# Optimization experiments

Measured on AMD Instinct MI355X. Metric: run time of the kernel, lower is better.

Reference implementation:

```python
import jax, jax.numpy as jnp
import numpy as np

C = 768      # n_embd
H = 12       # n_head
L = 6        # n_layer (per stack: base and head)
BS = 256     # block_size (per-stream length t)
B = 2        # batch
VU = 512     # vocab_size_up
VD = 512     # vocab_size_down
NM = 438     # n_music


def _ln(x, g, b, eps=1e-5):
    m = jnp.mean(x, -1, keepdims=True)
    v = jnp.mean((x - m) ** 2, -1, keepdims=True)
    return (x - m) * jax.lax.rsqrt(v + eps) * g + b


def _blocks(x, p, mask):
    # p: tuple of 16 stacked [L, ...] param arrays; scan over layers
    def body(x, lp):
        g1, b1, Wq, Bq, Wk, Bk, Wv, Bv, Wo, Bo, g2, b2, Wf, Bf, Wp, Bp = lp
        Bb, T, Cc = x.shape
        D = Cc // H
        h = _ln(x, g1, b1)
        q = (h @ Wq + Bq).reshape(Bb, T, H, D).transpose(0, 2, 1, 3)
        k = (h @ Wk + Bk).reshape(Bb, T, H, D).transpose(0, 2, 1, 3)
        v = (h @ Wv + Bv).reshape(Bb, T, H, D).transpose(0, 2, 1, 3)
        att = jnp.einsum('bhid,bhjd->bhij', q, k) * (1.0 / np.sqrt(D).astype(np.float32))
        att = jnp.where(mask, att, jnp.float32(-1e9))
        att = jax.nn.softmax(att, axis=-1)
        y = jnp.einsum('bhij,bhjd->bhid', att, v).transpose(0, 2, 1, 3).reshape(Bb, T, Cc)
        x = x + y @ Wo + Bo
        h2 = _ln(x, g2, b2)
        x = x + jax.nn.gelu(h2 @ Wf + Bf, approximate=False) @ Wp + Bp
        return x, None
    x, _ = jax.lax.scan(body, x, p)
    return x


def _forward(idx_up, idx_down, cond, tok_emb_up, tok_emb_down, pos_emb, cond_w, cond_b,
             base_p, head_p, ln_f_g, ln_f_b, head_up_w, head_down_w):
    t = idx_up.shape[1]
    te = jnp.concatenate([cond @ cond_w + cond_b, tok_emb_up[idx_up], tok_emb_down[idx_down]], axis=1)
    pe = jnp.concatenate([pos_emb[:, :t], pos_emb[:, BS:BS + t], pos_emb[:, 2 * BS:2 * BS + t]], axis=1)
    x = te + pe  # [B, 3t, C]
    tril = jnp.tril(jnp.ones((t, t), bool))
    mask = jnp.tile(tril, (3, 3))[None, None]  # 3x3 tiled block-causal mask [1,1,3t,3t]
    x = _blocks(x, base_p, mask)
    x = _blocks(x, head_p, mask)
    x = _ln(x, ln_f_g, ln_f_b)
    logits_up = x[:, t:2 * t] @ head_up_w
    logits_down = x[:, 2 * t:3 * t] @ head_down_w
    return logits_up, logits_down


def setup_inputs() -> dict:
    key = jax.random.key(0)
    ks = iter(jax.random.split(key, 100))
    def nrm(shape):
        return 0.02 * jax.random.normal(next(ks), shape, jnp.float32)
    inp = {
        'idx_up': jax.random.randint(next(ks), (B, BS), 0, VU),
        'idx_down': jax.random.randint(next(ks), (B, BS), 0, VD),
        'cond': jax.random.normal(next(ks), (B, BS, NM), jnp.float32),
        'tok_emb_up': nrm((VU, C)),
        'tok_emb_down': nrm((VD, C)),
        'pos_emb': nrm((1, 3 * BS, C)),
        'cond_w': nrm((NM, C)),
        'cond_b': jnp.zeros((C,), jnp.float32),
    }
    for pre in ('base_', 'head_'):
        inp[pre + 'ln1_g'] = jnp.ones((L, C), jnp.float32)
        inp[pre + 'ln1_b'] = jnp.zeros((L, C), jnp.float32)
        inp[pre + 'wq'] = nrm((L, C, C)); inp[pre + 'bq'] = jnp.zeros((L, C), jnp.float32)
        inp[pre + 'wk'] = nrm((L, C, C)); inp[pre + 'bk'] = jnp.zeros((L, C), jnp.float32)
        inp[pre + 'wv'] = nrm((L, C, C)); inp[pre + 'bv'] = jnp.zeros((L, C), jnp.float32)
        inp[pre + 'wo'] = nrm((L, C, C)); inp[pre + 'bo'] = jnp.zeros((L, C), jnp.float32)
        inp[pre + 'ln2_g'] = jnp.ones((L, C), jnp.float32)
        inp[pre + 'ln2_b'] = jnp.zeros((L, C), jnp.float32)
        inp[pre + 'fc_w'] = nrm((L, C, 4 * C)); inp[pre + 'fc_b'] = jnp.zeros((L, 4 * C), jnp.float32)
        inp[pre + 'pr_w'] = nrm((L, 4 * C, C)); inp[pre + 'pr_b'] = jnp.zeros((L, C), jnp.float32)
    inp['ln_f_g'] = jnp.ones((C,), jnp.float32)
    inp['ln_f_b'] = jnp.zeros((C,), jnp.float32)
    inp['head_up_w'] = nrm((C, VU))
    inp['head_down_w'] = nrm((C, VD))
    return inp


def reference(idx_up, idx_down, cond, tok_emb_up, tok_emb_down, pos_emb, cond_w, cond_b,
              base_ln1_g, base_ln1_b, base_wq, base_bq, base_wk, base_bk, base_wv, base_bv,
              base_wo, base_bo, base_ln2_g, base_ln2_b, base_fc_w, base_fc_b, base_pr_w, base_pr_b,
              head_ln1_g, head_ln1_b, head_wq, head_bq, head_wk, head_bk, head_wv, head_bv,
              head_wo, head_bo, head_ln2_g, head_ln2_b, head_fc_w, head_fc_b, head_pr_w, head_pr_b,
              ln_f_g, ln_f_b, head_up_w, head_down_w):
    base_p = (base_ln1_g, base_ln1_b, base_wq, base_bq, base_wk, base_bk, base_wv, base_bv,
              base_wo, base_bo, base_ln2_g, base_ln2_b, base_fc_w, base_fc_b, base_pr_w, base_pr_b)
    head_p = (head_ln1_g, head_ln1_b, head_wq, head_bq, head_wk, head_bk, head_wv, head_bv,
              head_wo, head_bo, head_ln2_g, head_ln2_b, head_fc_w, head_fc_b, head_pr_w, head_pr_b)
    return _forward(idx_up, idx_down, cond, tok_emb_up, tok_emb_down, pos_emb, cond_w, cond_b,
                    base_p, head_p, ln_f_g, ln_f_b, head_up_w, head_down_w)
```

## Files before the change

kernel.cpp:

```cpp
#include <hip/hip_runtime.h>
#include <cmath>

typedef unsigned short u16;
typedef __bf16 bf16x8 __attribute__((ext_vector_type(8)));
typedef float f32x4 __attribute__((ext_vector_type(4)));
typedef float f32x16 __attribute__((ext_vector_type(16)));
typedef u16 u16x4 __attribute__((ext_vector_type(4)));
typedef u16 u16x2 __attribute__((ext_vector_type(2)));

#define GLOAD16(g, l) __builtin_amdgcn_global_load_lds( \
    (const __attribute__((address_space(1))) unsigned int*)(g), \
    (__attribute__((address_space(3))) unsigned int*)(l), 16, 0, 0)

__device__ __forceinline__ u16 f2b(float f) {
  unsigned u = __builtin_bit_cast(unsigned, f);
  unsigned r = (u + 0x7fffu + ((u >> 16) & 1u)) >> 16;
  return (u16)r;
}

__device__ __forceinline__ int xcd_swz(int lin, int nwg) {
  int q = nwg >> 3, r = nwg & 7;
  int xcd = lin & 7, idx = lin >> 3;
  return xcd * q + (xcd < r ? xcd : r) + idx;
}

__device__ __forceinline__ void trans_tile(const float* __restrict__ W, u16* __restrict__ Wo,
                                           int K, int N, int Kp, int n0, int k0)
{
  __shared__ float t[32][33];
  int tx = threadIdx.x & 31, ty = threadIdx.x >> 5;
  #pragma unroll
  for (int i = 0; i < 4; ++i) {
    int k = k0 + ty + i * 8;
    t[ty + i * 8][tx] = (k < K) ? W[(long)k * N + n0 + tx] : 0.0f;
  }
  __syncthreads();
  #pragma unroll
  for (int i = 0; i < 2; ++i) {
    int p = threadIdx.x + 256 * i;
    int nl = p >> 4, kk = (p & 15) * 2;
    u16x2 o2; o2[0] = f2b(t[kk][nl]); o2[1] = f2b(t[kk + 1][nl]);
    *(u16x2*)(Wo + (long)(n0 + nl) * Kp + k0 + kk) = o2;
  }
}

__global__ __launch_bounds__(256)
void transall_k(const float* wq0, const float* wk0, const float* wv0, const float* wo0,
                const float* fc0, const float* pr0,
                const float* wq1, const float* wk1, const float* wv1, const float* wo1,
                const float* fc1, const float* pr1,
                const float* hu, const float* hd, const float* cw,
                u16* qkvt, u16* wot, u16* fct, u16* prt, u16* hutd, u16* cwt)
{
  int bid = blockIdx.x;
  const float* src; u16* dst; int K, N, Kp, t, tilesX;
  if (bid < 82944) {
    int l = bid / 6912, local = bid - l * 6912;
    int s = l / 6, li = l - s * 6;
    if (local < 1728) {
      int p = local / 576; t = local - p * 576;
      const float* base = (p == 0) ? (s ? wq1 : wq0) : (p == 1) ? (s ? wk1 : wk0) : (s ? wv1 : wv0);
      src = base + (size_t)li * 768 * 768;
      dst = qkvt + (size_t)l * 2304 * 768 + (size_t)p * 768 * 768;
      K = 768; N = 768; Kp = 768; tilesX = 24;
    } else if (local < 2304) {
      t = local - 1728;
      src = (s ? wo1 : wo0) + (size_t)li * 768 * 768;
      dst = wot + (size_t)l * 768 * 768;
      K = 768; N = 768; Kp = 768; tilesX = 24;
    } else if (local < 4608) {
      t = local - 2304;
      src = (s ? fc1 : fc0) + (size_t)li * 768 * 3072;
      dst = fct + (size_t)l * 3072 * 768;
      K = 768; N = 3072; Kp = 768; tilesX = 96;
    } else {
      t = local - 4608;
      src = (s ? pr1 : pr0) + (size_t)li * 3072 * 768;
      dst = prt + (size_t)l * 768 * 3072;
      K = 3072; N = 768; Kp = 3072; tilesX = 24;
    }
  } else {
    int e = bid - 82944;
    if (e < 384)      { t = e;       src = hu; dst = hutd;             K = 768; N = 512; Kp = 768; tilesX = 16; }
    else if (e < 768) { t = e - 384; src = hd; dst = hutd + 512 * 768; K = 768; N = 512; Kp = 768; tilesX = 16; }
    else              { t = e - 768; src = cw; dst = cwt;              K = 438; N = 768; Kp = 448; tilesX = 24; }
  }
  int n0 = (t % tilesX) * 32, k0 = (t / tilesX) * 32;
  trans_tile(src, dst, K, N, Kp, n0, k0);
}

__global__ __launch_bounds__(256)
void transw_k(const float* __restrict__ W, u16* __restrict__ Wt,
              int K, int N, int Kp, long sIn, long sOut)
{
  int l = blockIdx.z;
  trans_tile(W + (long)l * sIn, Wt + (long)l * sOut, K, N, Kp, blockIdx.x * 32, blockIdx.y * 32);
}

__global__ void biascat_k(const float* bq0, const float* bk0, const float* bv0,
                          const float* bq1, const float* bk1, const float* bv1, float* o)
{
  int idx = blockIdx.x * 256 + threadIdx.x;
  int c = idx % 2304, l = idx / 2304;
  int st = l / 6, li = l % 6;
  const float* src = (c < 768) ? (st ? bq1 : bq0) : (c < 1536) ? (st ? bk1 : bk0) : (st ? bv1 : bv0);
  o[idx] = src[li * 768 + (c % 768)];
}

__global__ void condcvt_k(const float* __restrict__ c, u16* __restrict__ o)
{
  int idx = blockIdx.x * 256 + threadIdx.x;
  int k = idx % 448, r = idx / 448;
  o[idx] = f2b(k < 438 ? c[r * 438 + k] : 0.0f);
}

__global__ void embed_k(const int* __restrict__ iu, const int* __restrict__ idn,
                        const float* __restrict__ teu, const float* __restrict__ ted,
                        const float* __restrict__ pe, float* __restrict__ x)
{
  int idx = blockIdx.x * 256 + threadIdx.x;
  int c4 = idx % 192; int rest = idx / 192;
  int tt = rest % 512; int b = rest / 512;
  int i = tt & 255; int s = tt >> 8;
  int tok = s ? idn[b * 256 + i] : iu[b * 256 + i];
  const float4* src = (const float4*)(s ? (ted + (long)tok * 768) : (teu + (long)tok * 768));
  int prow = 256 + s * 256 + i;
  float4 pv = ((const float4*)(pe + (long)prow * 768))[c4];
  float4 sv = src[c4];
  float4 ov; ov.x = sv.x + pv.x; ov.y = sv.y + pv.y; ov.z = sv.z + pv.z; ov.w = sv.w + pv.w;
  ((float4*)(x + ((long)b * 768 + prow) * 768))[c4] = ov;
}

template<int S, bool WX>
__global__ __launch_bounds__(256)
void lnred_k(const float* __restrict__ xin, const float* __restrict__ P,
             const float* __restrict__ bias, const float* __restrict__ gg,
             const float* __restrict__ bb, float* __restrict__ xout,
             u16* __restrict__ h)
{
  int row = blockIdx.x * 4 + (threadIdx.x >> 6);
  int lane = threadIdx.x & 63;
  long base = (long)row * 768;
  const float4* xr4 = (const float4*)(xin + base);
  float4 v[3]; float s = 0.0f;
  #pragma unroll
  for (int j = 0; j < 3; ++j) {
    int f = lane + 64 * j;
    float4 val = xr4[f];
    if (S > 0) {
      float4 bv = ((const float4*)bias)[f];
      val.x += bv.x; val.y += bv.y; val.z += bv.z; val.w += bv.w;
      #pragma unroll
      for (int si = 0; si < S; ++si) {
        float4 pv = ((const float4*)(P + (long)si * 1179648 + base))[f];
        val.x += pv.x; val.y += pv.y; val.z += pv.z; val.w += pv.w;
      }
    }
    if (WX) ((float4*)(xout + base))[f] = val;
    v[j] = val; s += val.x + val.y + val.z + val.w;
  }
  #pragma unroll
  for (int d = 1; d < 64; d <<= 1) s += __shfl_xor(s, d);
  float mean = s * (1.0f / 768.0f);
  float s2 = 0.0f;
  #pragma unroll
  for (int j = 0; j < 3; ++j) {
    float dx = v[j].x - mean, dy = v[j].y - mean, dz = v[j].z - mean, dw = v[j].w - mean;
    s2 += dx * dx + dy * dy + dz * dz + dw * dw;
  }
  #pragma unroll
  for (int d = 1; d < 64; d <<= 1) s2 += __shfl_xor(s2, d);
  float rstd = rsqrtf(s2 * (1.0f / 768.0f) + 1e-5f);
  u16* orow = h + base;
  #pragma unroll
  for (int j = 0; j < 3; ++j) {
    int f = lane + 64 * j;
    float4 gv = ((const float4*)gg)[f];
    float4 bv2 = ((const float4*)bb)[f];
    u16x4 pk;
    pk[0] = f2b((v[j].x - mean) * rstd * gv.x + bv2.x);
    pk[1] = f2b((v[j].y - mean) * rstd * gv.y + bv2.y);
    pk[2] = f2b((v[j].z - mean) * rstd * gv.z + bv2.z);
    pk[3] = f2b((v[j].w - mean) * rstd * gv.w + bv2.w);
    *(u16x4*)(orow + 4 * f) = pk;
  }
}

__global__ __launch_bounds__(256)
void headred_k(const float* __restrict__ HP, float* __restrict__ out)
{
  int i4 = blockIdx.x * 256 + threadIdx.x;
  int st = i4 >> 16, loc = i4 & 65535;
  int r = loc >> 7, c4 = loc & 127;
  const float4* basep = (const float4*)HP + (long)r * 256 + st * 128 + c4;
  float4 a = basep[0], b = basep[131072], c = basep[2 * 131072], d = basep[3 * 131072];
  float4 rr; rr.x = a.x + b.x + c.x + d.x; rr.y = a.y + b.y + c.y + d.y;
  rr.z = a.z + b.z + c.z + d.z; rr.w = a.w + b.w + c.w + d.w;
  ((float4*)out)[i4] = rr;
}

#define EPI_PLAIN 0
#define EPI_PE    1
#define EPI_QKV   2
#define EPI_GELU  4
#define EPI_PART  5
#define EPI_HEAD  6

template<int BM, int BN, int WM, int WN, int EPI, bool BIAS>
__global__ __launch_bounds__(256)
void gemm_k(const u16* __restrict__ A, const u16* __restrict__ Bt, const float* __restrict__ bias,
            float* outf, u16* outb, u16* qb, u16* kb, u16* vT, const float* aux,
            int M, int N, int Ks, int lda, int ldb, int ldc,
            int astr, int aoff, int cstr, int coff, int pstr)
{
  constexpr int NWC = BN / WN;
  constexpr int NT  = (BM / WM) * NWC * 64;
  constexpr int LCH = (BM + BN) * 8;
  constexpr int LPT = LCH / NT;
  constexpr int MR = WM / 32, NR = WN / 32;
  __shared__ alignas(16) u16 Sl[3][(BM + BN) * 64];

  const int tid = threadIdx.x;
  const int gx = gridDim.x, gy = gridDim.y;
  const int nwg = gx * gy * gridDim.z;
  const int lin = (blockIdx.z * gy + blockIdx.y) * gx + blockIdx.x;
  const int wg = xcd_swz(lin, nwg);
  const int bx = wg % gx, t1g = wg / gx;
  const int by = t1g % gy, bz = t1g / gy;
  const int m0 = bx * BM, n0 = by * BN;
  const int koff = bz * Ks;
  const int lane = tid & 63, w = tid >> 6;
  const int l31 = lane & 31, hl = lane >> 5;
  const int wr = w / NWC, wc = w % NWC;
  int aoffE = aoff;
  if constexpr (EPI == EPI_HEAD) aoffE += (by >= (int)(gy >> 1)) ? 256 : 0;

  const u16* gp[LPT]; int lbase[LPT];
  #pragma unroll
  for (int j = 0; j < LPT; ++j) {
    int c = tid + NT * j;
    int slot = c & 7;
    if (c < BM * 8) {
      int row = c >> 3;
      int se = (slot ^ (row & 7)) * 8;
      int am = m0 + row;
      gp[j] = A + (long)((am >> 8) * astr + aoffE + (am & 255)) * lda + koff + se;
    } else {
      int rb = c - BM * 8;
      int row = rb >> 3;
      int se = (slot ^ (row & 7)) * 8;
      gp[j] = Bt + (long)(n0 + row) * ldb + koff + se;
    }
    lbase[j] = w * 512 + NT * 8 * j;
  }

  int offA[4][MR], offB[4][NR];
  #pragma unroll
  for (int kst = 0; kst < 4; ++kst) {
    int s = 2 * kst + hl;
    #pragma unroll
    for (int mi = 0; mi < MR; ++mi) {
      int r = wr * WM + mi * 32 + l31;
      offA[kst][mi] = r * 128 + ((s ^ (r & 7)) << 4);
    }
    #pragma unroll
    for (int ni = 0; ni < NR; ++ni) {
      int r = wc * WN + ni * 32 + l31;
      offB[kst][ni] = BM * 128 + r * 128 + ((s ^ (r & 7)) << 4);
    }
  }

  f32x16 acc[MR][NR];
  #pragma unroll
  for (int mi = 0; mi < MR; ++mi)
  #pragma unroll
  for (int ni = 0; ni < NR; ++ni) acc[mi][ni] = f32x16{};

  auto STAGE = [&](int kt, int buf) {
    #pragma unroll
    for (int j = 0; j < LPT; ++j) GLOAD16(gp[j] + kt, &Sl[buf][lbase[j]]);
  };
  auto COMPUTE = [&](int buf) {
    const char* Sb = (const char*)&Sl[buf][0];
    #pragma unroll
    for (int kst = 0; kst < 4; ++kst) {
      bf16x8 a[MR], b[NR];
      #pragma unroll
      for (int mi = 0; mi < MR; ++mi) a[mi] = *(const bf16x8*)(Sb + offA[kst][mi]);
      #pragma unroll
      for (int ni = 0; ni < NR; ++ni) b[ni] = *(const bf16x8*)(Sb + offB[kst][ni]);
      #pragma unroll
      for (int mi = 0; mi < MR; ++mi)
      #pragma unroll
      for (int ni = 0; ni < NR; ++ni)
        acc[mi][ni] = __builtin_amdgcn_mfma_f32_32x32x16_bf16(a[mi], b[ni], acc[mi][ni], 0, 0, 0);
    }
  };

  const int nIter = Ks >> 6;
  STAGE(0, 0);
  if (nIter > 1) STAGE(64, 1);
  int cur = 0;
  for (int t = 0; t < nIter; ++t) {
    if (t + 1 < nIter) {
      if constexpr (LPT == 8)      asm volatile("s_waitcnt vmcnt(8)" ::: "memory");
      else if constexpr (LPT == 6) asm volatile("s_waitcnt vmcnt(6)" ::: "memory");
      else                         asm volatile("s_waitcnt vmcnt(4)" ::: "memory");
    } else {
      asm volatile("s_waitcnt vmcnt(0)" ::: "memory");
    }
    __builtin_amdgcn_s_barrier();
    if (t + 2 < nIter) {
      int nslot = cur + 2; if (nslot >= 3) nslot -= 3;
      STAGE((t + 2) << 6, nslot);
    }
    COMPUTE(cur);
    ++cur; if (cur == 3) cur = 0;
  }

  #pragma unroll
  for (int mi = 0; mi < MR; ++mi)
  #pragma unroll
  for (int ni = 0; ni < NR; ++ni) {
    f32x16 a = acc[mi][ni];
    int col = n0 + wc * WN + ni * 32 + l31;
    float bv = BIAS ? bias[col] : 0.0f;
    int mlb = m0 + wr * WM + mi * 32 + 4 * hl;
    if constexpr (EPI == EPI_QKV) {
      if (col >= 1536) {
        int c2 = col - 1536, hh = c2 >> 6, dd = c2 & 63;
        #pragma unroll
        for (int q = 0; q < 4; ++q) {
          int t0r = mlb + 8 * q;
          int bb2 = t0r >= 768 ? 1 : 0;
          int t0 = t0r - bb2 * 768;
          u16x4 pk;
          #pragma unroll
          for (int r = 0; r < 4; ++r) pk[r] = f2b(a[4 * q + r] + bv);
          *(u16x4*)(vT + (long)((bb2 * 12 + hh) * 64 + dd) * 768 + t0) = pk;
        }
      } else {
        u16* dst = (col < 768) ? (qb + col) : (kb + (col - 768));
        #pragma unroll
        for (int q = 0; q < 4; ++q)
        #pragma unroll
        for (int r = 0; r < 4; ++r) {
          int row = mlb + 8 * q + r;
          dst[(long)row * 768] = f2b(a[4 * q + r] + bv);
        }
      }
    } else {
      #pragma unroll
      for (int q = 0; q < 4; ++q)
      #pragma unroll
      for (int r = 0; r < 4; ++r) {
        int rg = mlb + 8 * q + r;
        long crow = (long)(rg >> 8) * cstr + coff + (rg & 255);
        float v = a[4 * q + r] + bv;
        if (EPI == EPI_PLAIN)      outf[crow * ldc + col] = v;
        else if (EPI == EPI_PE)    outf[crow * ldc + col] = v + aux[(long)(rg & 255) * 768 + col];
        else if (EPI == EPI_PART || EPI == EPI_HEAD)
                                   outf[(long)bz * pstr + (long)rg * ldc + col] = v;
        else if (EPI == EPI_GELU)  outb[crow * ldc + col] = f2b(0.5f * v * (1.0f + erff(v * 0.70710678f)));
      }
    }
  }
}

#define MFMA_BF16 __builtin_amdgcn_mfma_f32_16x16x32_bf16
__global__ __launch_bounds__(128)
void attn_k(const u16* __restrict__ qb, const u16* __restrict__ kb,
            const u16* __restrict__ vT, u16* __restrict__ y)
{
  __shared__ alignas(16) u16 Kl[3 * 4096];
  __shared__ alignas(16) u16 Vl[3 * 4096];
  __shared__ alignas(16) u16 Pl[2][16 * 72];
  const int gx = gridDim.x, gy = gridDim.y;
  const int nwg = gx * gy;
  const int lin = blockIdx.y * gx + blockIdx.x;
  const int wg = xcd_swz(lin, nwg);
  const int qt = wg % gx, bh = wg / gx;
  const int b = bh / 12, h = bh - b * 12;
  const int tid = threadIdx.x, w = tid >> 6, lane = tid & 63, l15 = lane & 15, g = lane >> 4;
  const int qrow = qt * 32 + w * 16 + l15;
  const int qm = qrow & 255;
  const int q0 = (qt * 32) & 255;
  const unsigned nw4 = (q0 >> 6) + 1;
  const int niter = 3 * nw4;
  const u16* qp = qb + (long)(b * 768 + qrow) * 768 + h * 64;
  bf16x8 qf0 = *(const bf16x8*)(qp + 8 * g);
  bf16x8 qf1 = *(const bf16x8*)(qp + 32 + 8 * g);
  f32x4 O0{}, O1{}, O2{}, O3{};
  float m_run = -1e30f, l_run = 0.0f;

  const u16* kp[4]; const u16* vp[4]; int ldsb[4];
  #pragma unroll
  for (int j = 0; j < 4; ++j) {
    int i = tid + 128 * j;
    int r = i >> 3, sl = ((i & 7) ^ (r & 7)) * 8;
    kp[j] = kb + (long)(b * 768 + r) * 768 + h * 64 + sl;
    vp[j] = vT + (long)(bh * 64 + r) * 768 + sl;
    ldsb[j] = (w + 2 * j) * 512;
  }

  auto STAGE = [&](int kt, int q) {
    u16* kd = Kl + q * 4096; u16* vd = Vl + q * 4096;
    #pragma unroll
    for (int j = 0; j < 4; ++j) GLOAD16(kp[j] + (long)kt * 64 * 768, kd + ldsb[j]);
    #pragma unroll
    for (int j = 0; j < 4; ++j) GLOAD16(vp[j] + kt * 64, vd + ldsb[j]);
  };
  auto MAP = [&](int it) {
    unsigned sb = (unsigned)it / nw4;
    return (int)(sb * 4 + ((unsigned)it - sb * nw4));
  };

  STAGE(MAP(0), 0);
  STAGE(MAP(1), 1);
  int cur = 0;
  for (int it = 0; it < niter; ++it) {
    if (it < niter - 1) asm volatile("s_waitcnt vmcnt(8)" ::: "memory");
    else                asm volatile("s_waitcnt vmcnt(0)" ::: "memory");
    __builtin_amdgcn_s_barrier();
    if (it + 2 < niter) STAGE(MAP(it + 2), cur == 0 ? 2 : cur - 1);
    const int kt = MAP(it);
    const char* Kb = (const char*)Kl + cur * 8192;
    const char* Vb = (const char*)Vl + cur * 8192;

    f32x4 s0{}, s1{}, s2{}, s3{};
    #pragma unroll
    for (int ks = 0; ks < 2; ++ks) {
      bf16x8 qf = ks ? qf1 : qf0;
      int sb = ((4 * ks + g) ^ (l15 & 7)) << 4;
      bf16x8 k0 = *(const bf16x8*)(Kb + (0  + l15) * 128 + sb);
      bf16x8 k1 = *(const bf16x8*)(Kb + (16 + l15) * 128 + sb);
      bf16x8 k2 = *(const bf16x8*)(Kb + (32 + l15) * 128 + sb);
      bf16x8 k3 = *(const bf16x8*)(Kb + (48 + l15) * 128 + sb);
      s0 = MFMA_BF16(k0, qf, s0, 0, 0, 0);
      s1 = MFMA_BF16(k1, qf, s1, 0, 0, 0);
      s2 = MFMA_BF16(k2, qf, s2, 0, 0, 0);
      s3 = MFMA_BF16(k3, qf, s3, 0, 0, 0);
    }
    float sv[16]; float tm = -1e30f;
    #pragma unroll
    for (int mt = 0; mt < 4; ++mt) {
      f32x4 sm4 = (mt == 0) ? s0 : (mt == 1) ? s1 : (mt == 2) ? s2 : s3;
      #pragma unroll
      for (int r = 0; r < 4; ++r) {
        int kg = kt * 64 + mt * 16 + 4 * g + r;
        float val = ((kg & 255) <= qm) ? sm4[r] * 0.125f : -1e30f;
        sv[mt * 4 + r] = val; tm = fmaxf(tm, val);
      }
    }
    tm = fmaxf(tm, __shfl_xor(tm, 16));
    tm = fmaxf(tm, __shfl_xor(tm, 32));
    float mn = fmaxf(m_run, tm);
    float alpha = __expf(m_run - mn);
    float ps = 0.0f; u16 pb16[16];
    #pragma unroll
    for (int j = 0; j < 16; ++j) {
      float p = (sv[j] <= -1e29f) ? 0.0f : __expf(sv[j] - mn);
      ps += p; pb16[j] = f2b(p);
    }
    ps += __shfl_xor(ps, 16); ps += __shfl_xor(ps, 32);
    l_run = l_run * alpha + ps; m_run = mn;
    float a0 = __shfl(alpha, 4 * g + 0);
    float a1 = __shfl(alpha, 4 * g + 1);
    float a2 = __shfl(alpha, 4 * g + 2);
    float a3 = __shfl(alpha, 4 * g + 3);
    #pragma unroll
    for (int mt = 0; mt < 4; ++mt) {
      u16x4 pk; pk[0] = pb16[4*mt]; pk[1] = pb16[4*mt+1]; pk[2] = pb16[4*mt+2]; pk[3] = pb16[4*mt+3];
      *(u16x4*)((char*)&Pl[w][0] + l15 * 144 + mt * 32 + 8 * g) = pk;
    }
    O0[0] *= a0; O0[1] *= a1; O0[2] *= a2; O0[3] *= a3;
    O1[0] *= a0; O1[1] *= a1; O1[2] *= a2; O1[3] *= a3;
    O2[0] *= a0; O2[1] *= a1; O2[2] *= a2; O2[3] *= a3;
    O3[0] *= a0; O3[1] *= a1; O3[2] *= a2; O3[3] *= a3;
    asm volatile("s_waitcnt lgkmcnt(0)" ::: "memory");
    __builtin_amdgcn_sched_barrier(0);
    #pragma unroll
    for (int ks = 0; ks < 2; ++ks) {
      bf16x8 pf = *(const bf16x8*)((const char*)&Pl[w][0] + l15 * 144 + 64 * ks + 16 * g);
      int sb = ((4 * ks + g) ^ (l15 & 7)) << 4;
      bf16x8 v0 = *(const bf16x8*)(Vb + (0  + l15) * 128 + sb);
      bf16x8 v1 = *(const bf16x8*)(Vb + (16 + l15) * 128 + sb);
      bf16x8 v2 = *(const bf16x8*)(Vb + (32 + l15) * 128 + sb);
      bf16x8 v3 = *(const bf16x8*)(Vb + (48 + l15) * 128 + sb);
      O0 = MFMA_BF16(pf, v0, O0, 0, 0, 0);
      O1 = MFMA_BF16(pf, v1, O1, 0, 0, 0);
      O2 = MFMA_BF16(pf, v2, O2, 0, 0, 0);
      O3 = MFMA_BF16(pf, v3, O3, 0, 0, 0);
    }
    cur = (cur == 2) ? 0 : cur + 1;
  }
  float n0i = 1.0f / __shfl(l_run, 4 * g + 0);
  float n1i = 1.0f / __shfl(l_run, 4 * g + 1);
  float n2i = 1.0f / __shfl(l_run, 4 * g + 2);
  float n3i = 1.0f / __shfl(l_run, 4 * g + 3);
  long yr = (long)(b * 768 + qt * 32 + w * 16 + 4 * g);
  #pragma unroll
  for (int ni = 0; ni < 4; ++ni) {
    f32x4 Ov = (ni == 0) ? O0 : (ni == 1) ? O1 : (ni == 2) ? O2 : O3;
    int c = h * 64 + ni * 16 + l15;
    y[(yr + 0) * 768 + c] = f2b(Ov[0] * n0i);
    y[(yr + 1) * 768 + c] = f2b(Ov[1] * n1i);
    y[(yr + 2) * 768 + c] = f2b(Ov[2] * n2i);
    y[(yr + 3) * 768 + c] = f2b(Ov[3] * n3i);
  }
}

extern "C" void kernel_launch(void* const* d_in, const int* in_sizes, int n_in,
                              void* d_out, int out_size, void* d_ws, size_t ws_size,
                              hipStream_t stream)
{
  (void)in_sizes; (void)n_in; (void)out_size;
  auto F = [&](int i){ return (const float*)d_in[i]; };
  const int* idx_up = (const int*)d_in[0];
  const int* idx_dn = (const int*)d_in[1];
  const float* cond = F(2);
  const float* teu = F(3);
  const float* ted = F(4);
  const float* pe  = F(5);
  const float* cw  = F(6);
  const float* cb  = F(7);
  float* outp = (float*)d_out;
  char* ws = (char*)d_ws;

  size_t o = 0;
  auto take = [&](size_t bytes){ void* p = ws + o; o += bytes; return p; };
  float* x    = (float*)take(4718592);
  u16*   h    = (u16*)take(2359296);
  u16*   qbuf = (u16*)take(2359296);
  u16*   kbuf = (u16*)take(2359296);
  u16*   vT   = (u16*)take(2359296);
  u16*   y    = (u16*)take(2359296);
  u16*   fca  = (u16*)take(9437184);
  u16*   xf   = (u16*)take(2359296);
  u16*   cbf  = (u16*)take(458752);
  float* qkvb = (float*)take(110592);
  u16*   hutd = (u16*)take(1572864);
  u16*   cwt  = (u16*)take(688128);
  float* P1   = (float*)take(9437184);
  float* P2   = (float*)take(9437184);
  float* HP   = (float*)take(8388608);
  const size_t WL = 14155776;
  bool up = (ws_size >= o + 12 * WL);
  size_t nsl = up ? 12 : 1;
  u16* qkvt = (u16*)(ws + o);
  u16* wot  = qkvt + nsl * 2304 * 768;
  u16* fct  = wot  + nsl * 768 * 768;
  u16* prt  = fct  + nsl * 3072 * 768;

  auto trans = [&](const float* src, u16* dst, int K, int N, int Kp, long sIn, long sOut, int nz){
    transw_k<<<dim3(N / 32, Kp / 32, nz), dim3(256), 0, stream>>>(src, dst, K, N, Kp, sIn, sOut);
  };

  if (up) {
    transall_k<<<dim3(84048), dim3(256), 0, stream>>>(
        F(10), F(12), F(14), F(16), F(20), F(22),
        F(26), F(28), F(30), F(32), F(36), F(38),
        F(42), F(43), cw,
        qkvt, wot, fct, prt, hutd, cwt);
  } else {
    trans(F(42), hutd, 768, 512, 768, 0, 0, 1);
    trans(F(43), hutd + 512 * 768, 768, 512, 768, 0, 0, 1);
    trans(cw,    cwt, 438, 768, 448, 0, 0, 1);
  }
  biascat_k<<<dim3(108), dim3(256), 0, stream>>>(F(11), F(13), F(15), F(27), F(29), F(31), qkvb);
  condcvt_k<<<dim3(896), dim3(256), 0, stream>>>(cond, cbf);
  embed_k<<<dim3(768), dim3(256), 0, stream>>>(idx_up, idx_dn, teu, ted, pe, x);
  gemm_k<64, 64, 32, 32, EPI_PE, true><<<dim3(8, 12, 1), dim3(256), 0, stream>>>(cbf, cwt, cb,
      x, nullptr, nullptr, nullptr, nullptr, pe,
      512, 768, 448, 448, 448, 768, 256, 0, 768, 0, 0);

  for (int l = 0; l < 12; ++l) {
    int s = l / 6, li = l % 6;
    u16* qkvt_l = qkvt + (up ? (size_t)l : 0) * 2304 * 768;
    u16* wot_l  = wot  + (up ? (size_t)l : 0) * 768 * 768;
    u16* fct_l  = fct  + (up ? (size_t)l : 0) * 3072 * 768;
    u16* prt_l  = prt  + (up ? (size_t)l : 0) * 768 * 3072;
    if (!up) {
      for (int p = 0; p < 3; ++p)
        trans(F(8 + 16*s + 2 + 2*p) + (size_t)li*768*768, qkvt_l + (size_t)p*768*768, 768, 768, 768, 0, 0, 1);
      trans(F(8 + 16*s + 8)  + (size_t)li*768*768,  wot_l, 768, 768, 768, 0, 0, 1);
      trans(F(8 + 16*s + 12) + (size_t)li*768*3072, fct_l, 768, 3072, 768, 0, 0, 1);
      trans(F(8 + 16*s + 14) + (size_t)li*3072*768, prt_l, 3072, 768, 3072, 0, 0, 1);
    }
    if (l == 0) {
      lnred_k<0, false><<<dim3(384), dim3(256), 0, stream>>>(x, nullptr, nullptr,
          F(8+16*s+0) + (size_t)li*768, F(8+16*s+1) + (size_t)li*768, nullptr, h);
    } else {
      int ps = (l - 1) / 6, pli = (l - 1) % 6;
      lnred_k<2, true><<<dim3(384), dim3(256), 0, stream>>>(x, P2,
          F(8+16*ps+15) + (size_t)pli*768,
          F(8+16*s+0) + (size_t)li*768, F(8+16*s+1) + (size_t)li*768, x, h);
    }
    gemm_k<128, 64, 32, 64, EPI_QKV, true><<<dim3(12, 36, 1), dim3(256), 0, stream>>>(h, qkvt_l, qkvb + (size_t)l*2304,
        nullptr, nullptr, qbuf, kbuf, vT, nullptr,
        1536, 2304, 768, 768, 768, 768, 256, 0, 256, 0, 0);
    attn_k<<<dim3(24, 24), dim3(128), 0, stream>>>(qbuf, kbuf, vT, y);
    gemm_k<128, 64, 32, 64, EPI_PART, false><<<dim3(12, 12, 2), dim3(256), 0, stream>>>(y, wot_l, nullptr,
        P1, nullptr, nullptr, nullptr, nullptr, nullptr,
        1536, 768, 384, 768, 768, 768, 256, 0, 256, 0, 1179648);
    lnred_k<2, true><<<dim3(384), dim3(256), 0, stream>>>(x, P1,
        F(8+16*s+9) + (size_t)li*768,
        F(8+16*s+10) + (size_t)li*768, F(8+16*s+11) + (size_t)li*768, x, h);
    gemm_k<128, 64, 32, 64, EPI_GELU, true><<<dim3(12, 48, 1), dim3(256), 0, stream>>>(h, fct_l, F(8+16*s+13) + (size_t)li*3072,
        nullptr, fca, nullptr, nullptr, nullptr, nullptr,
        1536, 3072, 768, 768, 768, 3072, 256, 0, 256, 0, 0);
    gemm_k<128, 64, 32, 64, EPI_PART, false><<<dim3(12, 12, 2), dim3(256), 0, stream>>>(fca, prt_l, nullptr,
        P2, nullptr, nullptr, nullptr, nullptr, nullptr,
        1536, 768, 1536, 3072, 3072, 768, 256, 0, 256, 0, 1179648);
  }
  lnred_k<2, false><<<dim3(384), dim3(256), 0, stream>>>(x, P2,
      F(8+16*1+15) + (size_t)5*768, F(40), F(41), nullptr, xf);
  gemm_k<64, 64, 32, 32, EPI_HEAD, false><<<dim3(8, 16, 4), dim3(256), 0, stream>>>(xf, hutd, nullptr,
      HP, nullptr, nullptr, nullptr, nullptr, nullptr,
      512, 1024, 192, 768, 768, 1024, 768, 256, 256, 0, 524288);
  headred_k<<<dim3(512), dim3(256), 0, stream>>>(HP, outp);
}
```

Before: 1.339 ms.

## Widen weight transpose tiles, vectorize cond convert, double-buffer GEMM LDS

The weight transpose kernel now works on 64x64 tiles with float4 loads and 8-wide bf16 stores, using a quarter of the blocks. This cuts per-block overhead and narrow memory transactions in the fp32-to-bf16 weight conversion that runs every call. The cond conversion kernel now writes 4 values per thread. The GEMM drops from three LDS stages to two and adds an extra barrier before each prefetch, which lowers LDS use so more blocks can fit per CU, at the cost of less load/compute overlap.

```diff
diff --git a/kernel.cpp b/kernel.cpp
--- a/kernel.cpp
+++ b/kernel.cpp
@@ -7,6 +7,7 @@
 typedef float f32x16 __attribute__((ext_vector_type(16)));
 typedef u16 u16x4 __attribute__((ext_vector_type(4)));
 typedef u16 u16x2 __attribute__((ext_vector_type(2)));
+typedef u16 u16x8 __attribute__((ext_vector_type(8)));
 
 #define GLOAD16(g, l) __builtin_amdgcn_global_load_lds( \
     (const __attribute__((address_space(1))) unsigned int*)(g), \
@@ -54,39 +55,60 @@
 {
   int bid = blockIdx.x;
   const float* src; u16* dst; int K, N, Kp, t, tilesX;
-  if (bid < 82944) {
-    int l = bid / 6912, local = bid - l * 6912;
+  if (bid < 20736) {
+    int l = bid / 1728, local = bid - l * 1728;
     int s = l / 6, li = l - s * 6;
-    if (local < 1728) {
-      int p = local / 576; t = local - p * 576;
+    if (local < 432) {
+      int p = local / 144; t = local - p * 144;
       const float* base = (p == 0) ? (s ? wq1 : wq0) : (p == 1) ? (s ? wk1 : wk0) : (s ? wv1 : wv0);
       src = base + (size_t)li * 768 * 768;
       dst = qkvt + (size_t)l * 2304 * 768 + (size_t)p * 768 * 768;
-      K = 768; N = 768; Kp = 768; tilesX = 24;
-    } else if (local < 2304) {
-      t = local - 1728;
+      K = 768; N = 768; Kp = 768; tilesX = 12;
+    } else if (local < 576) {
+      t = local - 432;
       src = (s ? wo1 : wo0) + (size_t)li * 768 * 768;
       dst = wot + (size_t)l * 768 * 768;
-      K = 768; N = 768; Kp = 768; tilesX = 24;
-    } else if (local < 4608) {
-      t = local - 2304;
+      K = 768; N = 768; Kp = 768; tilesX = 12;
+    } else if (local < 1152) {
+      t = local - 576;
       src = (s ? fc1 : fc0) + (size_t)li * 768 * 3072;
       dst = fct + (size_t)l * 3072 * 768;
-      K = 768; N = 3072; Kp = 768; tilesX = 96;
+      K = 768; N = 3072; Kp = 768; tilesX = 48;
     } else {
-      t = local - 4608;
+      t = local - 1152;
       src = (s ? pr1 : pr0) + (size_t)li * 3072 * 768;
       dst = prt + (size_t)l * 768 * 3072;
-      K = 3072; N = 768; Kp = 3072; tilesX = 24;
+      K = 3072; N = 768; Kp = 3072; tilesX = 12;
     }
   } else {
-    int e = bid - 82944;
-    if (e < 384)      { t = e;       src = hu; dst = hutd;             K = 768; N = 512; Kp = 768; tilesX = 16; }
-    else if (e < 768) { t = e - 384; src = hd; dst = hutd + 512 * 768; K = 768; N = 512; Kp = 768; tilesX = 16; }
-    else              { t = e - 768; src = cw; dst = cwt;              K = 438; N = 768; Kp = 448; tilesX = 24; }
-  }
-  int n0 = (t % tilesX) * 32, k0 = (t / tilesX) * 32;
-  trans_tile(src, dst, K, N, Kp, n0, k0);
+    int e = bid - 20736;
+    if (e < 96)       { t = e;       src = hu; dst = hutd;             K = 768; N = 512; Kp = 768; tilesX = 8; }
+    else if (e < 192) { t = e - 96;  src = hd; dst = hutd + 512 * 768; K = 768; N = 512; Kp = 768; tilesX = 8; }
+    else              { t = e - 192; src = cw; dst = cwt;              K = 438; N = 768; Kp = 448; tilesX = 12; }
+  }
+  int n0 = (t % tilesX) * 64, k0 = (t / tilesX) * 64;
+
+  __shared__ float tl[64][65];
+  const int tid = threadIdx.x;
+  const int c4 = (tid & 15) * 4, rbase = tid >> 4;
+  #pragma unroll
+  for (int p = 0; p < 4; ++p) {
+    int r = rbase + p * 16;
+    int k = k0 + r;
+    float4 v = make_float4(0.0f, 0.0f, 0.0f, 0.0f);
+    if (k < K) v = *(const float4*)(src + (long)k * N + n0 + c4);
+    tl[r][c4] = v.x; tl[r][c4 + 1] = v.y; tl[r][c4 + 2] = v.z; tl[r][c4 + 3] = v.w;
+  }
+  __syncthreads();
+  const int kg = (tid & 7) * 8, nbase = tid >> 3;
+  #pragma unroll
+  for (int p = 0; p < 2; ++p) {
+    int n = nbase + p * 32;
+    u16x8 pk;
+    #pragma unroll
+    for (int j = 0; j < 8; ++j) pk[j] = f2b(tl[kg + j][n]);
+    *(u16x8*)(dst + (long)(n0 + n) * Kp + k0 + kg) = pk;
+  }
 }
 
 __global__ __launch_bounds__(256)
@@ -110,8 +132,11 @@
 __global__ void condcvt_k(const float* __restrict__ c, u16* __restrict__ o)
 {
   int idx = blockIdx.x * 256 + threadIdx.x;
-  int k = idx % 448, r = idx / 448;
-  o[idx] = f2b(k < 438 ? c[r * 438 + k] : 0.0f);
+  int r = idx / 112, kk = (idx - r * 112) * 4;
+  u16x4 pk;
+  #pragma unroll
+  for (int i = 0; i < 4; ++i) { int k = kk + i; pk[i] = f2b(k < 438 ? c[r * 438 + k] : 0.0f); }
+  *(u16x4*)(o + r * 448 + kk) = pk;
 }
 
 __global__ void embed_k(const int* __restrict__ iu, const int* __restrict__ idn,
@@ -218,7 +243,7 @@
   constexpr int LCH = (BM + BN) * 8;
   constexpr int LPT = LCH / NT;
   constexpr int MR = WM / 32, NR = WN / 32;
-  __shared__ alignas(16) u16 Sl[3][(BM + BN) * 64];
+  __shared__ alignas(16) u16 Sl[2][(BM + BN) * 64];
 
   const int tid = threadIdx.x;
   const int gx = gridDim.x, gy = gridDim.y;
@@ -300,7 +325,6 @@
   const int nIter = Ks >> 6;
   STAGE(0, 0);
   if (nIter > 1) STAGE(64, 1);
-  int cur = 0;
   for (int t = 0; t < nIter; ++t) {
     if (t + 1 < nIter) {
       if constexpr (LPT == 8)      asm volatile("s_waitcnt vmcnt(8)" ::: "memory");
@@ -310,12 +334,11 @@
       asm volatile("s_waitcnt vmcnt(0)" ::: "memory");
     }
     __builtin_amdgcn_s_barrier();
+    COMPUTE(t & 1);
     if (t + 2 < nIter) {
-      int nslot = cur + 2; if (nslot >= 3) nslot -= 3;
-      STAGE((t + 2) << 6, nslot);
-    }
-    COMPUTE(cur);
-    ++cur; if (cur == 3) cur = 0;
+      __builtin_amdgcn_s_barrier();
+      STAGE((t + 2) << 6, t & 1);
+    }
   }
 
   #pragma unroll
@@ -557,7 +580,7 @@
   };
 
   if (up) {
-    transall_k<<<dim3(84048), dim3(256), 0, stream>>>(
+    transall_k<<<dim3(21012), dim3(256), 0, stream>>>(
         F(10), F(12), F(14), F(16), F(20), F(22),
         F(26), F(28), F(30), F(32), F(36), F(38),
         F(42), F(43), cw,
@@ -568,7 +591,7 @@
     trans(cw,    cwt, 438, 768, 448, 0, 0, 1);
   }
   biascat_k<<<dim3(108), dim3(256), 0, stream>>>(F(11), F(13), F(15), F(27), F(29), F(31), qkvb);
-  condcvt_k<<<dim3(896), dim3(256), 0, stream>>>(cond, cbf);
+  condcvt_k<<<dim3(224), dim3(256), 0, stream>>>(cond, cbf);
   embed_k<<<dim3(768), dim3(256), 0, stream>>>(idx_up, idx_dn, teu, ted, pe, x);
   gemm_k<64, 64, 32, 32, EPI_PE, true><<<dim3(8, 12, 1), dim3(256), 0, stream>>>(cbf, cwt, cb,
       x, nullptr, nullptr, nullptr, nullptr, pe,
```

Result: faster. 1.230 ms (-8.1%).
